# Performance work log

Hardware: AMD Instinct MI355X
Metric: run time of the kernel (lower is better)

The kernel has to match this reference:

```python
import jax, jax.numpy as jnp
import numpy as np

BS, NQ, NC = 64, 3000, 256
FH, FW, TOPK = 100, 100, 1500
INK_INF = jnp.float32(1e20)


def setup_inputs() -> dict:
    key = jax.random.key(0)
    k1, k2, k3 = jax.random.split(key, 3)
    u = jax.random.uniform(k1, (BS, NQ, 4), dtype=jnp.float32)
    # cx,cy in [0.25,0.75], w,h in [0,0.4] -> xyxy strictly inside [0,1]
    cxcy = 0.25 + 0.5 * u[..., :2]
    wh = 0.4 * u[..., 2:]
    output_coord = jnp.concatenate([cxcy, wh], axis=-1)
    output_class = jax.random.uniform(k2, (BS, NQ, NC), dtype=jnp.float32)
    # valid feature extent [valid_h, valid_w] per image (from ~mask cumsum in original)
    valid_feature_size = jax.random.randint(k3, (BS, 2), 50, FH + 1, dtype=jnp.int32)
    rows = jnp.arange(FH)[None, :, None]
    cols = jnp.arange(FW)[None, None, :]
    padding_mask = (rows >= valid_feature_size[:, 0][:, None, None]) | (
        cols >= valid_feature_size[:, 1][:, None, None]
    )  # (BS, FH, FW) bool, True = padded
    return {
        "output_coord": output_coord,
        "output_class": output_class,
        "valid_feature_size": valid_feature_size,
        "padding_mask": padding_mask,
        "feature_h": FH,
        "feature_w": FW,
        "topk": TOPK,
    }


def reference(output_coord, output_class, valid_feature_size, padding_mask,
              feature_h, feature_w, topk):
    bs = output_coord.shape[0]
    # scores = output_class.max(dim=-1); topk box select
    scores = jnp.max(output_class, axis=-1)                      # (bs, nq)
    _, topk_idx = jax.lax.top_k(scores, topk)                    # (bs, k)
    boxes = jnp.take_along_axis(output_coord, topk_idx[..., None], axis=1)  # (bs,k,4) cxcywh
    # box_cxcywh_to_xyxy
    cxcy, wh = boxes[..., :2], boxes[..., 2:]
    xyxy = jnp.concatenate([cxcy - 0.5 * wh, cxcy + 0.5 * wh], axis=-1)  # (bs,k,4)
    # valid_size.repeat(1,2) -> [vh, vw, vh, vw]
    vfs = valid_feature_size.astype(xyxy.dtype)
    scale = jnp.concatenate([vfs, vfs], axis=-1)[:, None, :]     # (bs,1,4)
    rng = jnp.floor(xyxy * scale).astype(jnp.int32)              # (bs,k,4)
    lx, ly, rx, ry = rng[..., 0], rng[..., 1], rng[..., 2], rng[..., 3]
    rows = jnp.arange(feature_h)
    cols = jnp.arange(feature_w)
    # per-box row/col membership; union over boxes via batched GEMM
    R = ((rows[None, None, :] >= ly[..., None]) & (rows[None, None, :] < ry[..., None])).astype(jnp.float32)  # (bs,k,h)
    C = ((cols[None, None, :] >= lx[..., None]) & (cols[None, None, :] < rx[..., None])).astype(jnp.float32)  # (bs,k,w)
    covered = jnp.einsum('bkh,bkw->bhw', R, C) > 0               # (bs,h,w)
    extra_mask = ~covered                                        # True outside every kept box
    # mask = extra_mask | padding_mask; float masked_fill(-INK_INF)
    full = extra_mask.reshape(bs, -1) | padding_mask.reshape(bs, -1)
    attn_mask = jnp.where(full, -INK_INF, jnp.float32(0.0))      # (bs, h*w)
    return attn_mask
```

## Files before the change

### kernel.cpp

```cpp
#include <hip/hip_runtime.h>

#define BS   64
#define NQ   3000
#define NC   256
#define FH   100
#define FW   100
#define TOPK 1500

__global__ __launch_bounds__(256) void scores_kernel(const float4* __restrict__ cls,
                                                     float* __restrict__ scores) {
    const int tid  = threadIdx.x;
    const int lane = tid & 63;
    const int wave = tid >> 6;
    const int row0 = blockIdx.x * 16 + wave * 4;
    const float4* p = cls + (size_t)row0 * (NC / 4) + lane;
    float4 a = p[0], b = p[64], c = p[128], d = p[192];
    float m0 = fmaxf(fmaxf(a.x, a.y), fmaxf(a.z, a.w));
    float m1 = fmaxf(fmaxf(b.x, b.y), fmaxf(b.z, b.w));
    float m2 = fmaxf(fmaxf(c.x, c.y), fmaxf(c.z, c.w));
    float m3 = fmaxf(fmaxf(d.x, d.y), fmaxf(d.z, d.w));
#pragma unroll
    for (int off = 32; off > 0; off >>= 1) {
        m0 = fmaxf(m0, __shfl_xor(m0, off, 64));
        m1 = fmaxf(m1, __shfl_xor(m1, off, 64));
        m2 = fmaxf(m2, __shfl_xor(m2, off, 64));
        m3 = fmaxf(m3, __shfl_xor(m3, off, 64));
    }
    if (lane < 4) {
        float m = (lane == 0) ? m0 : (lane == 1) ? m1 : (lane == 2) ? m2 : m3;
        scores[row0 + lane] = m;
    }
}

#define NSPLIT 8
#define NTM    512
#define QSLICE ((NQ + NSPLIT - 1) / NSPLIT)

__global__ __launch_bounds__(NTM) void raster_kernel(const float4* __restrict__ coord,
                                                     const int* __restrict__ vfs,
                                                     const float* __restrict__ scores,
                                                     unsigned* __restrict__ pcov) {
    __shared__ unsigned su[NQ];
    __shared__ int      hist[8][256];
    __shared__ unsigned cov[FH * 4];
    __shared__ int      eqlist[NQ];
    __shared__ int      wave_sum[4];
    __shared__ int      s_selbin, s_K, s_ecnt, s_qcut;

    const int part = blockIdx.x;
    const int b    = blockIdx.y;
    const int tid  = threadIdx.x;
    const int wid  = tid >> 6;

    for (int q = tid; q < NQ; q += NTM)
        su[q] = __float_as_uint(scores[b * NQ + q]);
    for (int i = tid; i < FH * 4; i += NTM) cov[i] = 0u;
    if (tid == 0) s_ecnt = 0;

    unsigned prefix = 0, pmask = 0;
    int K = TOPK;
#pragma unroll
    for (int p = 0; p < 4; ++p) {
        const int shift = 24 - 8 * p;
        for (int i = tid; i < 8 * 256; i += NTM) ((int*)hist)[i] = 0;
        __syncthreads();
        for (int q = tid; q < NQ; q += NTM) {
            unsigned u = su[q];
            if ((u & pmask) == prefix)
                atomicAdd(&hist[wid][(u >> shift) & 0xFF], 1);
        }
        __syncthreads();
        int x = 0, hx = 0, bin = 0;
        if (tid < 256) {
            bin = 255 - tid;
            hx = hist[0][bin] + hist[1][bin] + hist[2][bin] + hist[3][bin] +
                 hist[4][bin] + hist[5][bin] + hist[6][bin] + hist[7][bin];
            x = hx;
#pragma unroll
            for (int off = 1; off < 64; off <<= 1) {
                int y = __shfl_up(x, off, 64);
                if ((tid & 63) >= off) x += y;
            }
            if ((tid & 63) == 63) wave_sum[tid >> 6] = x;
        }
        __syncthreads();
        if (tid < 256) {
            int w = tid >> 6;
            for (int j = 0; j < w; ++j) x += wave_sum[j];
            int ge_incl = x;
            int ge_excl = x - hx;
            if (ge_incl >= K && ge_excl < K) {
                s_selbin = bin;
                s_K      = K - ge_excl;
            }
        }
        __syncthreads();
        prefix |= ((unsigned)s_selbin) << shift;
        pmask  |= (0xFFu << shift);
        K = s_K;
        __syncthreads();
    }
    const unsigned v      = prefix;
    const int      e_take = K;

    for (int q = tid; q < NQ; q += NTM)
        if (su[q] == v) { int i = atomicAdd(&s_ecnt, 1); eqlist[i] = q; }
    __syncthreads();
    const int E = s_ecnt;
    for (int i = tid; i < E; i += NTM) {
        int q = eqlist[i];
        int r = 0;
        for (int j = 0; j < E; ++j) r += (eqlist[j] < q) ? 1 : 0;
        if (r == e_take - 1) s_qcut = q + 1;
    }
    __syncthreads();
    const int qcut = s_qcut;

    const float s0 = (float)vfs[2 * b];
    const float s1 = (float)vfs[2 * b + 1];

    const int q0 = part * QSLICE;
    const int q1 = (q0 + QSLICE < NQ) ? (q0 + QSLICE) : NQ;
    for (int q = q0 + tid; q < q1; q += NTM) {
        unsigned u = su[q];
        if (u > v || (u == v && q < qcut)) {
            float4 c4 = coord[(size_t)b * NQ + q];
            float x1 = c4.x - 0.5f * c4.z, y1 = c4.y - 0.5f * c4.w;
            float x2 = c4.x + 0.5f * c4.z, y2 = c4.y + 0.5f * c4.w;
            int lx = (int)floorf(x1 * s0), ly = (int)floorf(y1 * s1);
            int rx = (int)floorf(x2 * s0), ry = (int)floorf(y2 * s1);
            int h0 = ly > 0 ? ly : 0, h1 = ry < FH ? ry : FH;
            int w0 = lx > 0 ? lx : 0, w1 = rx < FW ? rx : FW;
            if (h0 < h1 && w0 < w1) {
                unsigned m[4];
#pragma unroll
                for (int j = 0; j < 4; ++j) {
                    int lo = w0 - 32 * j; lo = lo < 0 ? 0 : lo;
                    int hi = w1 - 32 * j; hi = hi > 32 ? 32 : hi;
                    unsigned mm = 0u;
                    if (hi > lo) {
                        unsigned top = (hi >= 32) ? 0xFFFFFFFFu : ((1u << hi) - 1u);
                        unsigned bot = (lo <= 0) ? 0u : ((1u << lo) - 1u);
                        mm = top & ~bot;
                    }
                    m[j] = mm;
                }
                for (int h = h0; h < h1; ++h) {
#pragma unroll
                    for (int j = 0; j < 4; ++j)
                        if (m[j]) atomicOr(&cov[h * 4 + j], m[j]);
                }
            }
        }
    }
    __syncthreads();

    unsigned* dst = pcov + (size_t)(b * NSPLIT + part) * (FH * 4);
    for (int i = tid; i < FH * 4; i += NTM) dst[i] = cov[i];
}

__global__ __launch_bounds__(256) void emit_kernel(const unsigned* __restrict__ pcov,
                                                   const int* __restrict__ vfs,
                                                   float* __restrict__ out) {
    const int idx = blockIdx.x * 256 + threadIdx.x;
    if (idx >= BS * FH * FW) return;
    const int b    = idx / (FH * FW);
    const int cell = idx - b * (FH * FW);
    const int h    = cell / FW;
    const int w    = cell - h * FW;
    const unsigned* p = pcov + (size_t)b * NSPLIT * (FH * 4) + h * 4 + (w >> 5);
    unsigned acc = 0u;
#pragma unroll
    for (int s = 0; s < NSPLIT; ++s) acc |= p[s * (FH * 4)];
    const bool covered = (acc >> (w & 31)) & 1u;
    const bool pad     = (h >= vfs[2 * b]) || (w >= vfs[2 * b + 1]);
    out[idx] = (covered && !pad) ? 0.0f : -1e20f;
}

extern "C" void kernel_launch(void* const* d_in, const int* in_sizes, int n_in,
                              void* d_out, int out_size, void* d_ws, size_t ws_size,
                              hipStream_t stream) {
    const float4* coord = (const float4*)d_in[0];
    const float*  cls   = (const float*)d_in[1];
    const int*    vfs   = (const int*)d_in[2];
    float*    scores = (float*)d_ws;
    unsigned* pcov   = (unsigned*)((char*)d_ws + (size_t)BS * NQ * sizeof(float));
    float* out = (float*)d_out;

    const int rows = BS * NQ;
    scores_kernel<<<rows / 16, 256, 0, stream>>>((const float4*)cls, scores);
    raster_kernel<<<dim3(NSPLIT, BS), NTM, 0, stream>>>(coord, vfs, scores, pcov);
    emit_kernel<<<(BS * FH * FW) / 256, 256, 0, stream>>>(pcov, vfs, out);
}
```

Before: 301.3 us.

## Fuse emit into raster via last-block counter; aggregate histogram atomics per wave

Removes the separate emit kernel by having the last of the split blocks per image, found with a global atomic counter, OR the partial coverage masks and write the output. The counters are reset inside the scores kernel. The radix-select histogram now uses wave-level ballot aggregation to cut shared-memory atomic contention. The final pass also records candidates during the last histogram pass and scores are loaded vectorized. The tail emit work now runs on only 64 blocks, which may serialize; the threadfence and atomic handshake adds some latency.

After: 401.8 us. +33.4%, slower.

```diff
diff --git a/kernel.cpp b/kernel.cpp
--- a/kernel.cpp
+++ b/kernel.cpp
@@ -8,11 +8,13 @@
 #define TOPK 1500
 
 __global__ __launch_bounds__(256) void scores_kernel(const float4* __restrict__ cls,
-                                                     float* __restrict__ scores) {
+                                                     float* __restrict__ scores,
+                                                     int* __restrict__ counters) {
     const int tid  = threadIdx.x;
     const int lane = tid & 63;
     const int wave = tid >> 6;
     const int row0 = blockIdx.x * 16 + wave * 4;
+    if (blockIdx.x == 0 && tid < BS) counters[tid] = 0;
     const float4* p = cls + (size_t)row0 * (NC / 4) + lane;
     float4 a = p[0], b = p[64], c = p[128], d = p[192];
     float m0 = fmaxf(fmaxf(a.x, a.y), fmaxf(a.z, a.w));
@@ -39,23 +41,28 @@
 __global__ __launch_bounds__(NTM) void raster_kernel(const float4* __restrict__ coord,
                                                      const int* __restrict__ vfs,
                                                      const float* __restrict__ scores,
-                                                     unsigned* __restrict__ pcov) {
-    __shared__ unsigned su[NQ];
+                                                     unsigned* __restrict__ pcov,
+                                                     int* __restrict__ counters,
+                                                     float* __restrict__ out) {
+    __shared__ __align__(16) unsigned su[NQ];
     __shared__ int      hist[8][256];
     __shared__ unsigned cov[FH * 4];
     __shared__ int      eqlist[NQ];
     __shared__ int      wave_sum[4];
-    __shared__ int      s_selbin, s_K, s_ecnt, s_qcut;
+    __shared__ int      s_selbin, s_K, s_c24, s_qcut, s_last;
 
     const int part = blockIdx.x;
     const int b    = blockIdx.y;
     const int tid  = threadIdx.x;
     const int wid  = tid >> 6;
 
-    for (int q = tid; q < NQ; q += NTM)
-        su[q] = __float_as_uint(scores[b * NQ + q]);
+    {
+        const uint4* sp = (const uint4*)(scores + b * NQ);
+        uint4* sd = (uint4*)su;
+        for (int i = tid; i < NQ / 4; i += NTM) sd[i] = sp[i];
+    }
     for (int i = tid; i < FH * 4; i += NTM) cov[i] = 0u;
-    if (tid == 0) s_ecnt = 0;
+    if (tid == 0) s_c24 = 0;
 
     unsigned prefix = 0, pmask = 0;
     int K = TOPK;
@@ -65,9 +72,21 @@
         for (int i = tid; i < 8 * 256; i += NTM) ((int*)hist)[i] = 0;
         __syncthreads();
         for (int q = tid; q < NQ; q += NTM) {
-            unsigned u = su[q];
-            if ((u & pmask) == prefix)
-                atomicAdd(&hist[wid][(u >> shift) & 0xFF], 1);
+            unsigned u   = su[q];
+            bool     pr  = ((u & pmask) == prefix);
+            unsigned bin = (u >> shift) & 0xFF;
+            if (p == 3 && pr) eqlist[atomicAdd(&s_c24, 1)] = q;
+            unsigned long long act = __ballot(pr);
+            if (act) {
+                int leader = __ffsll((long long)act) - 1;
+                unsigned fb = (unsigned)__shfl((int)bin, leader, 64);
+                unsigned long long same = __ballot(pr && bin == fb);
+                if (same == act) {
+                    if ((tid & 63) == leader) atomicAdd(&hist[wid][fb], (int)__popcll(act));
+                } else if (pr) {
+                    atomicAdd(&hist[wid][bin], 1);
+                }
+            }
         }
         __syncthreads();
         int x = 0, hx = 0, bin = 0;
@@ -103,15 +122,17 @@
     const unsigned v      = prefix;
     const int      e_take = K;
 
-    for (int q = tid; q < NQ; q += NTM)
-        if (su[q] == v) { int i = atomicAdd(&s_ecnt, 1); eqlist[i] = q; }
-    __syncthreads();
-    const int E = s_ecnt;
-    for (int i = tid; i < E; i += NTM) {
+    const int C24 = s_c24;
+    for (int i = tid; i < C24; i += NTM) {
         int q = eqlist[i];
-        int r = 0;
-        for (int j = 0; j < E; ++j) r += (eqlist[j] < q) ? 1 : 0;
-        if (r == e_take - 1) s_qcut = q + 1;
+        if (su[q] == v) {
+            int r = 0;
+            for (int j = 0; j < C24; ++j) {
+                int qj = eqlist[j];
+                r += (su[qj] == v && qj < q) ? 1 : 0;
+            }
+            if (r == e_take - 1) s_qcut = q + 1;
+        }
     }
     __syncthreads();
     const int qcut = s_qcut;
@@ -155,26 +176,34 @@
     }
     __syncthreads();
 
-    unsigned* dst = pcov + (size_t)(b * NSPLIT + part) * (FH * 4);
-    for (int i = tid; i < FH * 4; i += NTM) dst[i] = cov[i];
-}
-
-__global__ __launch_bounds__(256) void emit_kernel(const unsigned* __restrict__ pcov,
-                                                   const int* __restrict__ vfs,
-                                                   float* __restrict__ out) {
-    const int idx = blockIdx.x * 256 + threadIdx.x;
-    if (idx >= BS * FH * FW) return;
-    const int b    = idx / (FH * FW);
-    const int cell = idx - b * (FH * FW);
-    const int h    = cell / FW;
-    const int w    = cell - h * FW;
-    const unsigned* p = pcov + (size_t)b * NSPLIT * (FH * 4) + h * 4 + (w >> 5);
-    unsigned acc = 0u;
-#pragma unroll
-    for (int s = 0; s < NSPLIT; ++s) acc |= p[s * (FH * 4)];
-    const bool covered = (acc >> (w & 31)) & 1u;
-    const bool pad     = (h >= vfs[2 * b]) || (w >= vfs[2 * b + 1]);
-    out[idx] = (covered && !pad) ? 0.0f : -1e20f;
+    {
+        unsigned* dst = pcov + (size_t)(b * NSPLIT + part) * (FH * 4);
+        for (int i = tid; i < FH * 4; i += NTM) dst[i] = cov[i];
+    }
+    __threadfence();
+    __syncthreads();
+    if (tid == 0) {
+        int prev = __hip_atomic_fetch_add(&counters[b], 1, __ATOMIC_ACQ_REL,
+                                          __HIP_MEMORY_SCOPE_AGENT);
+        s_last = (prev == NSPLIT - 1) ? 1 : 0;
+    }
+    __syncthreads();
+    if (s_last) {
+        __threadfence();
+        const int iv0 = vfs[2 * b], iv1 = vfs[2 * b + 1];
+        const unsigned* pb = pcov + (size_t)b * NSPLIT * (FH * 4);
+        for (int idx = tid; idx < FH * FW; idx += NTM) {
+            int h = idx / FW;
+            int w = idx - h * FW;
+            const unsigned* pp = pb + h * 4 + (w >> 5);
+            unsigned acc = 0u;
+#pragma unroll
+            for (int s = 0; s < NSPLIT; ++s) acc |= pp[s * (FH * 4)];
+            bool covered = (acc >> (w & 31)) & 1u;
+            bool pad = (h >= iv0) || (w >= iv1);
+            out[(size_t)b * (FH * FW) + idx] = (covered && !pad) ? 0.0f : -1e20f;
+        }
+    }
 }
 
 extern "C" void kernel_launch(void* const* d_in, const int* in_sizes, int n_in,
@@ -183,12 +212,13 @@
     const float4* coord = (const float4*)d_in[0];
     const float*  cls   = (const float*)d_in[1];
     const int*    vfs   = (const int*)d_in[2];
-    float*    scores = (float*)d_ws;
-    unsigned* pcov   = (unsigned*)((char*)d_ws + (size_t)BS * NQ * sizeof(float));
+    float*    scores   = (float*)d_ws;
+    unsigned* pcov     = (unsigned*)((char*)d_ws + (size_t)BS * NQ * sizeof(float));
+    int*      counters = (int*)((char*)d_ws + (size_t)BS * NQ * sizeof(float)
+                                            + (size_t)BS * NSPLIT * FH * 4 * sizeof(unsigned));
     float* out = (float*)d_out;
 
     const int rows = BS * NQ;
-    scores_kernel<<<rows / 16, 256, 0, stream>>>((const float4*)cls, scores);
-    raster_kernel<<<dim3(NSPLIT, BS), NTM, 0, stream>>>(coord, vfs, scores, pcov);
-    emit_kernel<<<(BS * FH * FW) / 256, 256, 0, stream>>>(pcov, vfs, out);
+    scores_kernel<<<rows / 16, 256, 0, stream>>>((const float4*)cls, scores, counters);
+    raster_kernel<<<dim3(NSPLIT, BS), NTM, 0, stream>>>(coord, vfs, scores, pcov, counters, out);
 }
```

## Replace per-row shared atomicOr rasterization with packed box list and per-word gather

Applied to the files above, without the earlier changes.

Selected boxes are now packed into a shared-memory list instead of each thread doing atomicOr over every covered row of a shared bitmap. Afterwards, 400 threads each own one (row, word) cell of the coverage bitmap and loop over all listed boxes to OR in their masks. The score load into shared memory is also vectorized to uint4. This aims to remove heavy LDS atomic contention and divergent per-box row loops, at the cost of a serial loop over roughly 190 boxes per thread, with the other threads of the block idle during that phase.

Result: slower. 323.6 us (+7.4%).

```diff
diff --git a/kernel.cpp b/kernel.cpp
--- a/kernel.cpp
+++ b/kernel.cpp
@@ -40,22 +40,24 @@
                                                      const int* __restrict__ vfs,
                                                      const float* __restrict__ scores,
                                                      unsigned* __restrict__ pcov) {
-    __shared__ unsigned su[NQ];
+    __shared__ __align__(16) unsigned su[NQ];
     __shared__ int      hist[8][256];
-    __shared__ unsigned cov[FH * 4];
     __shared__ int      eqlist[NQ];
+    __shared__ unsigned boxlist[QSLICE];
     __shared__ int      wave_sum[4];
-    __shared__ int      s_selbin, s_K, s_ecnt, s_qcut;
+    __shared__ int      s_selbin, s_K, s_ecnt, s_qcut, s_nbox;
 
     const int part = blockIdx.x;
     const int b    = blockIdx.y;
     const int tid  = threadIdx.x;
     const int wid  = tid >> 6;
 
-    for (int q = tid; q < NQ; q += NTM)
-        su[q] = __float_as_uint(scores[b * NQ + q]);
-    for (int i = tid; i < FH * 4; i += NTM) cov[i] = 0u;
-    if (tid == 0) s_ecnt = 0;
+    {
+        const uint4* sp = (const uint4*)(scores + b * NQ);
+        uint4* sd = (uint4*)su;
+        for (int i = tid; i < NQ / 4; i += NTM) sd[i] = sp[i];
+    }
+    if (tid == 0) { s_ecnt = 0; s_nbox = 0; }
 
     unsigned prefix = 0, pmask = 0;
     int K = TOPK;
@@ -132,31 +134,32 @@
             int h0 = ly > 0 ? ly : 0, h1 = ry < FH ? ry : FH;
             int w0 = lx > 0 ? lx : 0, w1 = rx < FW ? rx : FW;
             if (h0 < h1 && w0 < w1) {
-                unsigned m[4];
-#pragma unroll
-                for (int j = 0; j < 4; ++j) {
-                    int lo = w0 - 32 * j; lo = lo < 0 ? 0 : lo;
-                    int hi = w1 - 32 * j; hi = hi > 32 ? 32 : hi;
-                    unsigned mm = 0u;
-                    if (hi > lo) {
-                        unsigned top = (hi >= 32) ? 0xFFFFFFFFu : ((1u << hi) - 1u);
-                        unsigned bot = (lo <= 0) ? 0u : ((1u << lo) - 1u);
-                        mm = top & ~bot;
-                    }
-                    m[j] = mm;
-                }
-                for (int h = h0; h < h1; ++h) {
-#pragma unroll
-                    for (int j = 0; j < 4; ++j)
-                        if (m[j]) atomicOr(&cov[h * 4 + j], m[j]);
-                }
+                unsigned pk = (unsigned)h0 | ((unsigned)h1 << 8) |
+                              ((unsigned)w0 << 16) | ((unsigned)w1 << 24);
+                boxlist[atomicAdd(&s_nbox, 1)] = pk;
             }
         }
     }
     __syncthreads();
 
-    unsigned* dst = pcov + (size_t)(b * NSPLIT + part) * (FH * 4);
-    for (int i = tid; i < FH * 4; i += NTM) dst[i] = cov[i];
+    const int nbox = s_nbox;
+    if (tid < FH * 4) {
+        const int h = tid >> 2, j = tid & 3;
+        unsigned acc = 0u;
+        for (int i = 0; i < nbox; ++i) {
+            unsigned pk = boxlist[i];
+            int h0 = (int)(pk & 0xFF), h1 = (int)((pk >> 8) & 0xFF);
+            int w0 = (int)((pk >> 16) & 0xFF), w1 = (int)((pk >> 24) & 0xFF);
+            int lo = w0 - 32 * j; lo = lo < 0 ? 0 : lo;
+            int hi = w1 - 32 * j; hi = hi > 32 ? 32 : hi;
+            unsigned top = (hi >= 32) ? 0xFFFFFFFFu : ((1u << (hi > 0 ? hi : 0)) - 1u);
+            unsigned bot = (lo <= 0) ? 0u : ((1u << lo) - 1u);
+            unsigned mm  = (hi > lo) ? (top & ~bot) : 0u;
+            unsigned act = (h >= h0 && h < h1) ? 0xFFFFFFFFu : 0u;
+            acc |= mm & act;
+        }
+        pcov[(size_t)(b * NSPLIT + part) * (FH * 4) + tid] = acc;
+    }
 }
 
 __global__ __launch_bounds__(256) void emit_kernel(const unsigned* __restrict__ pcov,
```
